# Kernel optimization log

Hardware: AMD Instinct MI355X
Metric: run time of the kernel (lower is better)

The kernel has to match this reference:

```python
import jax, jax.numpy as jnp
import numpy as np

WS = 25          # window_size
THRESHOLD = 3.5  # default threshold in find_low_quality_regions


def _conv1d_gelu(x, w, b, pad):
    # x: (N, C_in, L), w: (C_out, C_in, K) -> gelu(conv(x) + b), SAME length
    y = jax.lax.conv_general_dilated(
        x, w, window_strides=(1,), padding=[(pad, pad)],
        dimension_numbers=("NCH", "OIH", "NCH"))
    return jax.nn.gelu(y + b[None, :, None], approximate=False)


def setup_inputs() -> dict:
    key = jax.random.key(0)
    ks = jax.random.split(key, 12)
    B, T, D, H = 8, 25000, 256, 128
    s = 0.05
    return {
        "latents": jax.random.normal(ks[0], (B, T, D), jnp.float32),
        "conv0_w": jax.random.normal(ks[1], (H, D, 7), jnp.float32) * s,
        "conv0_b": jax.random.normal(ks[2], (H,), jnp.float32) * s,
        "conv1_w": jax.random.normal(ks[3], (H, H, 5), jnp.float32) * s,
        "conv1_b": jax.random.normal(ks[4], (H,), jnp.float32) * s,
        "conv2_w": jax.random.normal(ks[5], (H, H, 5), jnp.float32) * s,
        "conv2_b": jax.random.normal(ks[6], (H,), jnp.float32) * s,
        "head_w1": jax.random.normal(ks[7], (H, H), jnp.float32) * s,
        "head_b1": jax.random.normal(ks[8], (H,), jnp.float32) * s,
        "head_w2": jax.random.normal(ks[9], (1, H), jnp.float32) * s,
        "head_b2": jax.random.normal(ks[10], (1,), jnp.float32) * s,
    }


def reference(latents, conv0_w, conv0_b, conv1_w, conv1_b, conv2_w, conv2_b,
              head_w1, head_b1, head_w2, head_b2):
    B, T, D = latents.shape
    nw = (T - WS) // WS + 1  # number of non-overlapping windows
    # (B, nw, WS, D) -> (B*nw, D, WS): batch all windows through the critic
    x = latents[:, :nw * WS].reshape(B, nw, WS, D).reshape(B * nw, WS, D)
    x = jnp.transpose(x, (0, 2, 1))  # NCH
    x = _conv1d_gelu(x, conv0_w, conv0_b, pad=3)
    x = _conv1d_gelu(x, conv1_w, conv1_b, pad=2)
    x = _conv1d_gelu(x, conv2_w, conv2_b, pad=2)
    feat = x.mean(axis=2)  # AdaptiveAvgPool1d(1) -> (B*nw, H)
    h = jax.nn.gelu(feat @ head_w1.T + head_b1, approximate=False)
    score = jax.nn.sigmoid(h @ head_w2.T + head_b2)[:, 0] * 5.0  # (B*nw,)
    scores = score.reshape(B, nw).mean(axis=0)  # critic(window).mean() per window
    low_quality = scores < THRESHOLD  # windows the loop would append as regions
    return scores, low_quality
```

## Files before the change

### kernel.cpp

```cpp
#include <hip/hip_runtime.h>
#include <math.h>

#define BATCH 8
#define T_LEN 25000
#define NW    1000
#define WS    25
#define D0    256
#define H     128

typedef __bf16 bf16;
typedef bf16 bf16x8 __attribute__((ext_vector_type(8)));
typedef bf16 bf16x4 __attribute__((ext_vector_type(4)));
typedef float f32x4 __attribute__((ext_vector_type(4)));

__device__ __forceinline__ float gelu_fast(float x) {
    float y = 0.7978845608f * x * (1.0f + 0.044715f * x * x);
    float e = __expf(2.0f * y);
    float t = 1.0f - 2.0f * __builtin_amdgcn_rcpf(e + 1.0f);
    return 0.5f * x * (1.0f + t);
}

__device__ __forceinline__ void repack_one(const float* __restrict__ w,
                                           bf16* __restrict__ dst, int idx,
                                           int Cin, int K, int KSn) {
    int j    = idx & 7;
    int lane = (idx >> 3) & 63;
    int mt   = (idx >> 9) & 7;
    int ks   = (idx >> 12) % KSn;
    int k    = idx / (4096 * KSn);
    int co = mt * 16 + (lane & 15);
    int ci = ks * 32 + (lane >> 4) * 8 + j;
    dst[idx] = (bf16)w[(co * Cin + ci) * K + k];
}

__global__ void prep_kernel(const float* __restrict__ c0w, const float* __restrict__ c1w,
                            const float* __restrict__ c2w, const float* __restrict__ hw1,
                            bf16* __restrict__ p0, bf16* __restrict__ p1,
                            bf16* __restrict__ p2, bf16* __restrict__ hw1b) {
    int t = blockIdx.x * 256 + threadIdx.x;
    if (t < 229376) {
        repack_one(c0w, p0, t, 256, 7, 8);
    } else if (t < 311296) {
        repack_one(c1w, p1, t - 229376, 128, 5, 4);
    } else if (t < 393216) {
        repack_one(c2w, p2, t - 311296, 128, 5, 4);
    } else if (t < 409600) {
        int i = t - 393216;
        hw1b[i] = (bf16)hw1[i];
    }
}

#define XT_LD 264
#define A_LD  136
#define OFF_A2   33456
#define OFF_FEAT 70752
#define OFF_H    72800
#define SMEM_BYTES 74848

#define ISSUE_A(buf, base) \
    asm volatile("global_load_dwordx4 %0, %4, off\n\t"              \
                 "global_load_dwordx4 %1, %4, off offset:1024\n\t"  \
                 "global_load_dwordx4 %2, %4, off offset:2048\n\t"  \
                 "global_load_dwordx4 %3, %4, off offset:3072"      \
                 : "=&v"((buf)[0]), "=&v"((buf)[1]), "=&v"((buf)[2]), "=&v"((buf)[3]) \
                 : "v"(base))

#define WAIT_A(buf, Nlit) do {                                       \
    asm volatile("s_waitcnt vmcnt(" #Nlit ")"                        \
                 : "+v"((buf)[0]), "+v"((buf)[1]), "+v"((buf)[2]), "+v"((buf)[3])); \
    __builtin_amdgcn_sched_barrier(0);                               \
} while (0)

__device__ __forceinline__ void lds_barrier() {
    asm volatile("s_waitcnt lgkmcnt(0)" ::: "memory");
    __builtin_amdgcn_s_barrier();
}

template<int NS, int KSN, int LD>
__device__ __forceinline__ void conv_phase_pipe(const char* __restrict__ Abase,
                                                const bf16* __restrict__ bbase,
                                                int rowoff, f32x4 (&acc)[4][2]) {
    bf16x8 a[3][4];
    bf16x8 bb[2][2];
    ISSUE_A(a[0], Abase);
    ISSUE_A(a[1], Abase + 8192);
    lds_barrier();
    {
        const bf16* pB = bbase + rowoff * LD;
        bb[0][0] = *(const bf16x8*)pB;
        bb[0][1] = *(const bf16x8*)(pB + 16 * LD);
    }
    #pragma unroll
    for (int s = 0; s < NS; ++s) {
        const int cur = s & 1, nxt = cur ^ 1;
        const int ap = s % 3;
        if (s + 2 < NS)
            ISSUE_A(a[(s + 2) % 3], Abase + (size_t)(s + 2) * 8192);
        if (s + 2 < NS)      WAIT_A(a[ap], 8);
        else if (s + 1 < NS) WAIT_A(a[ap], 4);
        else                 WAIT_A(a[ap], 0);
        if (s + 1 < NS) {
            const int k1 = (s + 1) / KSN, ks1 = (s + 1) % KSN;
            const bf16* pB = bbase + (k1 + rowoff) * LD + ks1 * 32;
            bb[nxt][0] = *(const bf16x8*)pB;
            bb[nxt][1] = *(const bf16x8*)(pB + 16 * LD);
        }
        acc[0][0] = __builtin_amdgcn_mfma_f32_16x16x32_bf16(a[ap][0], bb[cur][0], acc[0][0], 0, 0, 0);
        acc[0][1] = __builtin_amdgcn_mfma_f32_16x16x32_bf16(a[ap][0], bb[cur][1], acc[0][1], 0, 0, 0);
        acc[1][0] = __builtin_amdgcn_mfma_f32_16x16x32_bf16(a[ap][1], bb[cur][0], acc[1][0], 0, 0, 0);
        acc[1][1] = __builtin_amdgcn_mfma_f32_16x16x32_bf16(a[ap][1], bb[cur][1], acc[1][1], 0, 0, 0);
        acc[2][0] = __builtin_amdgcn_mfma_f32_16x16x32_bf16(a[ap][2], bb[cur][0], acc[2][0], 0, 0, 0);
        acc[2][1] = __builtin_amdgcn_mfma_f32_16x16x32_bf16(a[ap][2], bb[cur][1], acc[2][1], 0, 0, 0);
        acc[3][0] = __builtin_amdgcn_mfma_f32_16x16x32_bf16(a[ap][3], bb[cur][0], acc[3][0], 0, 0, 0);
        acc[3][1] = __builtin_amdgcn_mfma_f32_16x16x32_bf16(a[ap][3], bb[cur][1], acc[3][1], 0, 0, 0);
    }
}

__global__ __launch_bounds__(512, 4)
void critic_kernel(const float* __restrict__ lat,
                   const bf16* __restrict__ p0, const float* __restrict__ b0,
                   const bf16* __restrict__ p1, const float* __restrict__ b1,
                   const bf16* __restrict__ p2, const float* __restrict__ b2,
                   const bf16* __restrict__ hw1b, const float* __restrict__ hb1,
                   const float* __restrict__ hw2, const float* __restrict__ hb2,
                   float* __restrict__ scores_tmp) {
    __shared__ __align__(16) char smem[SMEM_BYTES];
    bf16  (*xT)[XT_LD]  = (bf16(*)[XT_LD])smem;
    bf16  (*a1T)[A_LD]  = (bf16(*)[A_LD])smem;
    bf16  (*a2T)[A_LD]  = (bf16(*)[A_LD])(smem + OFF_A2);
    float* feat = (float*)(smem + OFF_FEAT);
    float* hbuf = (float*)(smem + OFF_H);

    const int tid = threadIdx.x;
    const int bx  = blockIdx.x;
    const int b   = bx / (NW / 4);
    const int wi  = bx % (NW / 4);
    const int w0  = 4 * wi;

    {
        const float4* src4 = (const float4*)(lat + ((size_t)b * T_LEN + (size_t)w0 * WS) * D0);
        #pragma unroll
        for (int it = 0; it < 13; ++it) {
            int g = tid + it * 512;
            if (g < 6400) {
                int l = g >> 6, c0 = (g & 63) * 4;
                int win = l / 25, lr = l - win * 25;
                int r = 31 * win + lr + 3;
                float4 v = src4[g];
                bf16x4 o = {(bf16)v.x, (bf16)v.y, (bf16)v.z, (bf16)v.w};
                *(bf16x4*)&xT[r][c0] = o;
            }
        }
        bf16x4 z4 = {};
        #pragma unroll
        for (int it = 0; it < 3; ++it) {
            int i = tid + it * 512;
            int rr = i >> 6, c0 = (i & 63) * 4;
            int j = rr / 6, t6 = rr - 6 * j;
            int r = 31 * j + ((t6 < 3) ? t6 : t6 + 25);
            *(bf16x4*)&xT[r][c0] = z4;
        }
    }

    const int lane = tid & 63, wv = tid >> 6;
    const int win = wv & 3, mtg = wv >> 2;
    const int m = lane & 15, q = lane >> 4;
    const bf16* xb  = &xT[m][q * 8];
    const bf16* a1b = &a1T[m][q * 8];
    const char* A0 = (const char*)p0 + (size_t)(mtg * 256 + lane) * 16;
    const char* A1 = (const char*)p1 + (size_t)(mtg * 256 + lane) * 16;
    const char* A2 = (const char*)p2 + (size_t)(mtg * 256 + lane) * 16;

    f32x4 acc[4][2] = {};
    conv_phase_pipe<56, 8, XT_LD>(A0, xb, 31 * win, acc);
    __syncthreads();
    {
        bf16x4 z4 = {};
        #pragma unroll
        for (int it = 0; it < 2; ++it) {
            int i = tid + it * 512;
            int arr = i >> 9, rr = (i >> 5) & 15, c0 = (i & 31) * 4;
            int j = rr >> 2, t4 = rr & 3;
            int r = 29 * j + ((t4 < 2) ? t4 : t4 + 25);
            if (arr == 0) *(bf16x4*)&a1T[r][c0] = z4;
            else          *(bf16x4*)&a2T[r][c0] = z4;
        }
    }
    #pragma unroll
    for (int i = 0; i < 4; ++i) {
        int co0 = (mtg * 4 + i) * 16 + q * 4;
        f32x4 bv = *(const f32x4*)&b0[co0];
        #pragma unroll
        for (int nt = 0; nt < 2; ++nt) {
            int l = nt * 16 + m;
            if (l < 25) {
                bf16x4 v;
                #pragma unroll
                for (int r = 0; r < 4; ++r)
                    v[r] = (bf16)gelu_fast(acc[i][nt][r] + bv[r]);
                *(bf16x4*)&a1T[l + 2 + 29 * win][co0] = v;
            }
        }
    }

    f32x4 c1[4][2] = {};
    conv_phase_pipe<20, 4, A_LD>(A1, a1b, 29 * win, c1);
    #pragma unroll
    for (int i = 0; i < 4; ++i) {
        int co0 = (mtg * 4 + i) * 16 + q * 4;
        f32x4 bv = *(const f32x4*)&b1[co0];
        #pragma unroll
        for (int nt = 0; nt < 2; ++nt) {
            int l = nt * 16 + m;
            if (l < 25) {
                bf16x4 v;
                #pragma unroll
                for (int r = 0; r < 4; ++r)
                    v[r] = (bf16)gelu_fast(c1[i][nt][r] + bv[r]);
                *(bf16x4*)&a2T[l + 2 + 29 * win][co0] = v;
            }
        }
    }

    f32x4 c2[4][2] = {};
    conv_phase_pipe<20, 4, A_LD>(A2, &a2T[m][q * 8], 29 * win, c2);
    #pragma unroll
    for (int i = 0; i < 4; ++i) {
        int co0 = (mtg * 4 + i) * 16 + q * 4;
        f32x4 bv = *(const f32x4*)&b2[co0];
        f32x4 pool;
        #pragma unroll
        for (int r = 0; r < 4; ++r) {
            float s  = gelu_fast(c2[i][0][r] + bv[r]);
            float g1 = gelu_fast(c2[i][1][r] + bv[r]);
            s += (m < 9) ? g1 : 0.0f;
            s += __shfl_xor(s, 1);
            s += __shfl_xor(s, 2);
            s += __shfl_xor(s, 4);
            s += __shfl_xor(s, 8);
            pool[r] = s * 0.04f;
        }
        if (m == 0) *(f32x4*)&feat[win * 128 + co0] = pool;
    }
    __syncthreads();

    {
        int wb = tid >> 7, co = tid & 127;
        const bf16x8* row = (const bf16x8*)(hw1b + co * H);
        const float* f0 = feat + wb * 128;
        float a0h = hb1[co];
        #pragma unroll
        for (int jv = 0; jv < 16; ++jv) {
            bf16x8 w8 = row[jv];
            #pragma unroll
            for (int u = 0; u < 8; ++u)
                a0h += (float)w8[u] * f0[jv * 8 + u];
        }
        hbuf[wb * 128 + co] = gelu_fast(a0h);
    }
    __syncthreads();

    if (tid < 256) {
        int win2 = tid >> 6, j = tid & 63;
        const float* hb = hbuf + win2 * 128;
        float p = hw2[j] * hb[j] + hw2[j + 64] * hb[j + 64];
        #pragma unroll
        for (int off = 32; off > 0; off >>= 1) p += __shfl_down(p, off);
        if (j == 0) {
            float z = p + hb2[0];
            scores_tmp[b * NW + w0 + win2] = 5.0f / (1.0f + expf(-z));
        }
    }
}

__global__ void finalize_kernel(const float* __restrict__ tmp, float* __restrict__ out) {
    int w = blockIdx.x * 256 + threadIdx.x;
    if (w < NW) {
        float s = 0.0f;
        #pragma unroll
        for (int b = 0; b < BATCH; ++b) s += tmp[b * NW + w];
        s *= 0.125f;
        out[w] = s;
        out[NW + w] = (s < 3.5f) ? 1.0f : 0.0f;
    }
}

extern "C" void kernel_launch(void* const* d_in, const int* in_sizes, int n_in,
                              void* d_out, int out_size, void* d_ws, size_t ws_size,
                              hipStream_t stream) {
    const float* lat  = (const float*)d_in[0];
    const float* c0w  = (const float*)d_in[1];
    const float* c0b  = (const float*)d_in[2];
    const float* c1w  = (const float*)d_in[3];
    const float* c1b  = (const float*)d_in[4];
    const float* c2w  = (const float*)d_in[5];
    const float* c2b  = (const float*)d_in[6];
    const float* hw1  = (const float*)d_in[7];
    const float* hb1  = (const float*)d_in[8];
    const float* hw2  = (const float*)d_in[9];
    const float* hb2  = (const float*)d_in[10];

    bf16* p0   = (bf16*)d_ws;
    bf16* p1   = (bf16*)((char*)d_ws + 458752);
    bf16* p2   = (bf16*)((char*)d_ws + 622592);
    bf16* hw1b = (bf16*)((char*)d_ws + 786432);
    float* tmp = (float*)((char*)d_ws + 819200);

    prep_kernel<<<1600, 256, 0, stream>>>(c0w, c1w, c2w, hw1, p0, p1, p2, hw1b);
    critic_kernel<<<BATCH * (NW / 4), 512, 0, stream>>>(lat, p0, c0b, p1, c1b, p2, c2b,
                                                        hw1b, hb1, hw2, hb2, tmp);
    finalize_kernel<<<4, 256, 0, stream>>>(tmp, (float*)d_out);
}
```

Before: 498.4 us.

## Give each wave two windows to reuse conv weight fragments, halving block size

The critic kernel now runs 256 threads per block instead of 512. Each wave computes two windows at once with a 4x4 accumulator tile, so every weight fragment loaded from global memory feeds twice as many MFMAs. The latent staging, padding zeroing, epilogues and head MLP are re-indexed so each thread covers two windows. This cuts per-block weight traffic and load-issue overhead, at the cost of more registers per thread and fewer resident waves to hide latency.

```diff
diff --git a/kernel.cpp b/kernel.cpp
--- a/kernel.cpp
+++ b/kernel.cpp
@@ -79,16 +79,19 @@
 template<int NS, int KSN, int LD>
 __device__ __forceinline__ void conv_phase_pipe(const char* __restrict__ Abase,
                                                 const bf16* __restrict__ bbase,
-                                                int rowoff, f32x4 (&acc)[4][2]) {
+                                                int r0, int r1, f32x4 (&acc)[4][4]) {
     bf16x8 a[3][4];
-    bf16x8 bb[2][2];
+    bf16x8 bb[2][4];
     ISSUE_A(a[0], Abase);
     ISSUE_A(a[1], Abase + 8192);
     lds_barrier();
     {
-        const bf16* pB = bbase + rowoff * LD;
-        bb[0][0] = *(const bf16x8*)pB;
-        bb[0][1] = *(const bf16x8*)(pB + 16 * LD);
+        const bf16* pB0 = bbase + r0 * LD;
+        const bf16* pB1 = bbase + r1 * LD;
+        bb[0][0] = *(const bf16x8*)(pB0);
+        bb[0][1] = *(const bf16x8*)(pB0 + 16 * LD);
+        bb[0][2] = *(const bf16x8*)(pB1);
+        bb[0][3] = *(const bf16x8*)(pB1 + 16 * LD);
     }
     #pragma unroll
     for (int s = 0; s < NS; ++s) {
@@ -101,22 +104,25 @@
         else                 WAIT_A(a[ap], 0);
         if (s + 1 < NS) {
             const int k1 = (s + 1) / KSN, ks1 = (s + 1) % KSN;
-            const bf16* pB = bbase + (k1 + rowoff) * LD + ks1 * 32;
-            bb[nxt][0] = *(const bf16x8*)pB;
-            bb[nxt][1] = *(const bf16x8*)(pB + 16 * LD);
-        }
-        acc[0][0] = __builtin_amdgcn_mfma_f32_16x16x32_bf16(a[ap][0], bb[cur][0], acc[0][0], 0, 0, 0);
-        acc[0][1] = __builtin_amdgcn_mfma_f32_16x16x32_bf16(a[ap][0], bb[cur][1], acc[0][1], 0, 0, 0);
-        acc[1][0] = __builtin_amdgcn_mfma_f32_16x16x32_bf16(a[ap][1], bb[cur][0], acc[1][0], 0, 0, 0);
-        acc[1][1] = __builtin_amdgcn_mfma_f32_16x16x32_bf16(a[ap][1], bb[cur][1], acc[1][1], 0, 0, 0);
-        acc[2][0] = __builtin_amdgcn_mfma_f32_16x16x32_bf16(a[ap][2], bb[cur][0], acc[2][0], 0, 0, 0);
-        acc[2][1] = __builtin_amdgcn_mfma_f32_16x16x32_bf16(a[ap][2], bb[cur][1], acc[2][1], 0, 0, 0);
-        acc[3][0] = __builtin_amdgcn_mfma_f32_16x16x32_bf16(a[ap][3], bb[cur][0], acc[3][0], 0, 0, 0);
-        acc[3][1] = __builtin_amdgcn_mfma_f32_16x16x32_bf16(a[ap][3], bb[cur][1], acc[3][1], 0, 0, 0);
-    }
-}
-
-__global__ __launch_bounds__(512, 4)
+            const int o = k1 * LD + ks1 * 32;
+            const bf16* pB0 = bbase + r0 * LD + o;
+            const bf16* pB1 = bbase + r1 * LD + o;
+            bb[nxt][0] = *(const bf16x8*)(pB0);
+            bb[nxt][1] = *(const bf16x8*)(pB0 + 16 * LD);
+            bb[nxt][2] = *(const bf16x8*)(pB1);
+            bb[nxt][3] = *(const bf16x8*)(pB1 + 16 * LD);
+        }
+        #pragma unroll
+        for (int i = 0; i < 4; ++i) {
+            acc[i][0] = __builtin_amdgcn_mfma_f32_16x16x32_bf16(a[ap][i], bb[cur][0], acc[i][0], 0, 0, 0);
+            acc[i][1] = __builtin_amdgcn_mfma_f32_16x16x32_bf16(a[ap][i], bb[cur][1], acc[i][1], 0, 0, 0);
+            acc[i][2] = __builtin_amdgcn_mfma_f32_16x16x32_bf16(a[ap][i], bb[cur][2], acc[i][2], 0, 0, 0);
+            acc[i][3] = __builtin_amdgcn_mfma_f32_16x16x32_bf16(a[ap][i], bb[cur][3], acc[i][3], 0, 0, 0);
+        }
+    }
+}
+
+__global__ __launch_bounds__(256, 2)
 void critic_kernel(const float* __restrict__ lat,
                    const bf16* __restrict__ p0, const float* __restrict__ b0,
                    const bf16* __restrict__ p1, const float* __restrict__ b1,
@@ -140,21 +146,19 @@
     {
         const float4* src4 = (const float4*)(lat + ((size_t)b * T_LEN + (size_t)w0 * WS) * D0);
         #pragma unroll
-        for (int it = 0; it < 13; ++it) {
-            int g = tid + it * 512;
-            if (g < 6400) {
-                int l = g >> 6, c0 = (g & 63) * 4;
-                int win = l / 25, lr = l - win * 25;
-                int r = 31 * win + lr + 3;
-                float4 v = src4[g];
-                bf16x4 o = {(bf16)v.x, (bf16)v.y, (bf16)v.z, (bf16)v.w};
-                *(bf16x4*)&xT[r][c0] = o;
-            }
+        for (int it = 0; it < 25; ++it) {
+            int g = tid + it * 256;
+            int l = g >> 6, c0 = (g & 63) * 4;
+            int win = l / 25, lr = l - win * 25;
+            int r = 31 * win + lr + 3;
+            float4 v = src4[g];
+            bf16x4 o = {(bf16)v.x, (bf16)v.y, (bf16)v.z, (bf16)v.w};
+            *(bf16x4*)&xT[r][c0] = o;
         }
         bf16x4 z4 = {};
         #pragma unroll
-        for (int it = 0; it < 3; ++it) {
-            int i = tid + it * 512;
+        for (int it = 0; it < 6; ++it) {
+            int i = tid + it * 256;
             int rr = i >> 6, c0 = (i & 63) * 4;
             int j = rr / 6, t6 = rr - 6 * j;
             int r = 31 * j + ((t6 < 3) ? t6 : t6 + 25);
@@ -163,22 +167,22 @@
     }
 
     const int lane = tid & 63, wv = tid >> 6;
-    const int win = wv & 3, mtg = wv >> 2;
+    const int wp = wv & 1, mtg = wv >> 1;
     const int m = lane & 15, q = lane >> 4;
     const bf16* xb  = &xT[m][q * 8];
     const bf16* a1b = &a1T[m][q * 8];
-    const char* A0 = (const char*)p0 + (size_t)(mtg * 256 + lane) * 16;
-    const char* A1 = (const char*)p1 + (size_t)(mtg * 256 + lane) * 16;
-    const char* A2 = (const char*)p2 + (size_t)(mtg * 256 + lane) * 16;
-
-    f32x4 acc[4][2] = {};
-    conv_phase_pipe<56, 8, XT_LD>(A0, xb, 31 * win, acc);
+    const char* A0 = (const char*)p0 + mtg * 4096 + lane * 16;
+    const char* A1 = (const char*)p1 + mtg * 4096 + lane * 16;
+    const char* A2 = (const char*)p2 + mtg * 4096 + lane * 16;
+
+    f32x4 acc[4][4] = {};
+    conv_phase_pipe<56, 8, XT_LD>(A0, xb, 31 * (2 * wp), 31 * (2 * wp + 1), acc);
     __syncthreads();
     {
         bf16x4 z4 = {};
         #pragma unroll
-        for (int it = 0; it < 2; ++it) {
-            int i = tid + it * 512;
+        for (int it = 0; it < 4; ++it) {
+            int i = tid + it * 256;
             int arr = i >> 9, rr = (i >> 5) & 15, c0 = (i & 31) * 4;
             int j = rr >> 2, t4 = rr & 3;
             int r = 29 * j + ((t4 < 2) ? t4 : t4 + 25);
@@ -191,56 +195,68 @@
         int co0 = (mtg * 4 + i) * 16 + q * 4;
         f32x4 bv = *(const f32x4*)&b0[co0];
         #pragma unroll
-        for (int nt = 0; nt < 2; ++nt) {
-            int l = nt * 16 + m;
-            if (l < 25) {
-                bf16x4 v;
-                #pragma unroll
-                for (int r = 0; r < 4; ++r)
-                    v[r] = (bf16)gelu_fast(acc[i][nt][r] + bv[r]);
-                *(bf16x4*)&a1T[l + 2 + 29 * win][co0] = v;
+        for (int wq = 0; wq < 2; ++wq) {
+            int win = 2 * wp + wq;
+            #pragma unroll
+            for (int nt = 0; nt < 2; ++nt) {
+                int l = nt * 16 + m;
+                if (l < 25) {
+                    bf16x4 v;
+                    #pragma unroll
+                    for (int r = 0; r < 4; ++r)
+                        v[r] = (bf16)gelu_fast(acc[i][2 * wq + nt][r] + bv[r]);
+                    *(bf16x4*)&a1T[l + 2 + 29 * win][co0] = v;
+                }
             }
         }
     }
 
-    f32x4 c1[4][2] = {};
-    conv_phase_pipe<20, 4, A_LD>(A1, a1b, 29 * win, c1);
+    f32x4 c1[4][4] = {};
+    conv_phase_pipe<20, 4, A_LD>(A1, a1b, 29 * (2 * wp), 29 * (2 * wp + 1), c1);
     #pragma unroll
     for (int i = 0; i < 4; ++i) {
         int co0 = (mtg * 4 + i) * 16 + q * 4;
         f32x4 bv = *(const f32x4*)&b1[co0];
         #pragma unroll
-        for (int nt = 0; nt < 2; ++nt) {
-            int l = nt * 16 + m;
-            if (l < 25) {
-                bf16x4 v;
-                #pragma unroll
-                for (int r = 0; r < 4; ++r)
-                    v[r] = (bf16)gelu_fast(c1[i][nt][r] + bv[r]);
-                *(bf16x4*)&a2T[l + 2 + 29 * win][co0] = v;
+        for (int wq = 0; wq < 2; ++wq) {
+            int win = 2 * wp + wq;
+            #pragma unroll
+            for (int nt = 0; nt < 2; ++nt) {
+                int l = nt * 16 + m;
+                if (l < 25) {
+                    bf16x4 v;
+                    #pragma unroll
+                    for (int r = 0; r < 4; ++r)
+                        v[r] = (bf16)gelu_fast(c1[i][2 * wq + nt][r] + bv[r]);
+                    *(bf16x4*)&a2T[l + 2 + 29 * win][co0] = v;
+                }
             }
         }
     }
 
-    f32x4 c2[4][2] = {};
-    conv_phase_pipe<20, 4, A_LD>(A2, &a2T[m][q * 8], 29 * win, c2);
+    f32x4 c2[4][4] = {};
+    conv_phase_pipe<20, 4, A_LD>(A2, &a2T[m][q * 8], 29 * (2 * wp), 29 * (2 * wp + 1), c2);
     #pragma unroll
     for (int i = 0; i < 4; ++i) {
         int co0 = (mtg * 4 + i) * 16 + q * 4;
         f32x4 bv = *(const f32x4*)&b2[co0];
-        f32x4 pool;
-        #pragma unroll
-        for (int r = 0; r < 4; ++r) {
-            float s  = gelu_fast(c2[i][0][r] + bv[r]);
-            float g1 = gelu_fast(c2[i][1][r] + bv[r]);
-            s += (m < 9) ? g1 : 0.0f;
-            s += __shfl_xor(s, 1);
-            s += __shfl_xor(s, 2);
-            s += __shfl_xor(s, 4);
-            s += __shfl_xor(s, 8);
-            pool[r] = s * 0.04f;
-        }
-        if (m == 0) *(f32x4*)&feat[win * 128 + co0] = pool;
+        #pragma unroll
+        for (int wq = 0; wq < 2; ++wq) {
+            int win = 2 * wp + wq;
+            f32x4 pool;
+            #pragma unroll
+            for (int r = 0; r < 4; ++r) {
+                float s  = gelu_fast(c2[i][2 * wq][r] + bv[r]);
+                float g1 = gelu_fast(c2[i][2 * wq + 1][r] + bv[r]);
+                s += (m < 9) ? g1 : 0.0f;
+                s += __shfl_xor(s, 1);
+                s += __shfl_xor(s, 2);
+                s += __shfl_xor(s, 4);
+                s += __shfl_xor(s, 8);
+                pool[r] = s * 0.04f;
+            }
+            if (m == 0) *(f32x4*)&feat[win * 128 + co0] = pool;
+        }
     }
     __syncthreads();
 
@@ -248,27 +264,32 @@
         int wb = tid >> 7, co = tid & 127;
         const bf16x8* row = (const bf16x8*)(hw1b + co * H);
         const float* f0 = feat + wb * 128;
-        float a0h = hb1[co];
+        const float* f1 = feat + (wb + 2) * 128;
+        float a0h = hb1[co], a1h = a0h;
         #pragma unroll
         for (int jv = 0; jv < 16; ++jv) {
             bf16x8 w8 = row[jv];
             #pragma unroll
-            for (int u = 0; u < 8; ++u)
-                a0h += (float)w8[u] * f0[jv * 8 + u];
+            for (int u = 0; u < 8; ++u) {
+                float wf = (float)w8[u];
+                a0h += wf * f0[jv * 8 + u];
+                a1h += wf * f1[jv * 8 + u];
+            }
         }
         hbuf[wb * 128 + co] = gelu_fast(a0h);
+        hbuf[(wb + 2) * 128 + co] = gelu_fast(a1h);
     }
     __syncthreads();
 
-    if (tid < 256) {
-        int win2 = tid >> 6, j = tid & 63;
-        const float* hb = hbuf + win2 * 128;
+    {
+        int win = tid >> 6, j = tid & 63;
+        const float* hb = hbuf + win * 128;
         float p = hw2[j] * hb[j] + hw2[j + 64] * hb[j + 64];
         #pragma unroll
         for (int off = 32; off > 0; off >>= 1) p += __shfl_down(p, off);
         if (j == 0) {
             float z = p + hb2[0];
-            scores_tmp[b * NW + w0 + win2] = 5.0f / (1.0f + expf(-z));
+            scores_tmp[b * NW + w0 + win] = 5.0f / (1.0f + expf(-z));
         }
     }
 }
@@ -307,7 +328,7 @@
     float* tmp = (float*)((char*)d_ws + 819200);
 
     prep_kernel<<<1600, 256, 0, stream>>>(c0w, c1w, c2w, hw1, p0, p1, p2, hw1b);
-    critic_kernel<<<BATCH * (NW / 4), 512, 0, stream>>>(lat, p0, c0b, p1, c1b, p2, c2b,
+    critic_kernel<<<BATCH * (NW / 4), 256, 0, stream>>>(lat, p0, c0b, p1, c1b, p2, c2b,
                                                         hw1b, hb1, hw2, hb2, tmp);
     finalize_kernel<<<4, 256, 0, stream>>>(tmp, (float*)d_out);
 }
```

Measured after the change: 437.5 us. 1.14x faster.
